# Kernel optimization log

Measured on AMD Instinct MI355X. Metric: run time of the kernel, lower is better.

Reference implementation:

```python
import jax, jax.numpy as jnp
import numpy as np


def setup_inputs() -> dict:
    key = jax.random.key(0)
    k1, k2 = jax.random.split(key)
    B, S, D = 32, 1024, 384
    MAX_MEL_LEN = 8192  # >= max possible sum of durations (7*1024)
    x = jax.random.normal(k1, (B, S, D), dtype=jnp.float32)
    duration = jax.random.randint(k2, (B, S), 0, 8, dtype=jnp.int32)
    return {"x": x, "duration": duration, "max_mel_len": MAX_MEL_LEN}


def reference(x, duration, max_mel_len):
    # x: (B, S, D) float, duration: (B, S) int, max_mel_len: python int
    B, S, D = x.shape
    csum = jnp.cumsum(duration, axis=1)          # (B, S) inclusive cumsum
    mel_len = csum[:, -1]                        # (B,) expanded length per sample
    t = jnp.arange(max_mel_len, dtype=csum.dtype)  # (T,) output frame indices
    # frame t maps to token i where csum[i-1] <= t < csum[i]; side='right'
    # correctly skips zero-duration tokens (repeated csum values)
    idx = jax.vmap(lambda c: jnp.searchsorted(c, t, side='right'))(csum)  # (B, T)
    idx = jnp.clip(idx, 0, S - 1)
    out = jnp.take_along_axis(x, idx[:, :, None], axis=1)  # (B, T, D) gather
    mask = t[None, :] < mel_len[:, None]                   # (B, T) pad mask
    out = out * mask[:, :, None].astype(x.dtype)
    return out, mel_len.astype(jnp.int64)
```

## Files before the change

### kernel.cpp

```cpp
#include <hip/hip_runtime.h>


#define BATCH 32
#define SRC_S 1024
#define DIM   384
#define ROWS  32
#define C4    (DIM / 4)
#define NXCD  8

typedef float f32x4 __attribute__((ext_vector_type(4)));

__global__ void lr_scan_idx_kernel(const int* __restrict__ duration,
                                   int* __restrict__ idx_g,
                                   float* __restrict__ mel_out, int T) {
    __shared__ int wsum[16];
    const int b = blockIdx.x;
    const int tid = threadIdx.x;
    const int lane = tid & 63;
    const int wid = tid >> 6;
    const int d = duration[b * SRC_S + tid];

    int v = d;
    #pragma unroll
    for (int off = 1; off < 64; off <<= 1) {
        const int n = __shfl_up(v, off, 64);
        if (lane >= off) v += n;
    }
    if (lane == 63) wsum[wid] = v;
    __syncthreads();
    if (tid < 16) {
        int w = wsum[tid];
        #pragma unroll
        for (int off = 1; off < 16; off <<= 1) {
            const int n = __shfl_up(w, off, 64);
            if (tid >= off) w += n;
        }
        wsum[tid] = w;
    }
    __syncthreads();
    const int wbase = (wid == 0) ? 0 : wsum[wid - 1];
    const int end = wbase + v;
    const int start = end - d;
    const int mel_len = wsum[15];

    int* __restrict__ ib = idx_g + (size_t)b * T;
    for (int t = start; t < end; ++t) ib[t] = tid;
    for (int t = mel_len + tid; t < T; t += SRC_S) ib[t] = -1;

    if (tid == SRC_S - 1) mel_out[b] = (float)mel_len;
}

__global__ __launch_bounds__(256)
void lr_gather_kernel(const f32x4* __restrict__ x4,
                      const int* __restrict__ idx_g,
                      f32x4* __restrict__ out4, int T) {
    const int l = blockIdx.x;
    const int xcd = l & (NXCD - 1);
    const int j = l >> 3;
    const int b = xcd + NXCD * (j >> 8);
    const int t0 = (j & 255) * ROWS;
    const int tid = threadIdx.x;

    const int* __restrict__ ib = idx_g + (size_t)b * T + t0;
    const f32x4* __restrict__ xb = x4 + (size_t)b * SRC_S * C4;
    f32x4* __restrict__ ob = out4 + ((size_t)b * T + t0) * C4;

    #pragma unroll
    for (int k = 0; k < (ROWS * C4) / 256; ++k) {
        const int i = tid + k * 256;
        const int row = i / C4;
        const int col = i - row * C4;
        const int sidx = ib[row];
        f32x4 v = (f32x4)(0.f);
        if (sidx >= 0) v = xb[(size_t)sidx * C4 + col];
        __builtin_nontemporal_store(v, &ob[i]);
    }
}

extern "C" void kernel_launch(void* const* d_in, const int* in_sizes, int n_in,
                              void* d_out, int out_size, void* d_ws, size_t ws_size,
                              hipStream_t stream) {
    const float* x = (const float*)d_in[0];
    const int* duration = (const int*)d_in[1];
    const int T = (out_size - BATCH) / (BATCH * DIM);

    int* idx_g = (int*)d_ws;
    float* out = (float*)d_out;
    float* mel_out = out + (size_t)BATCH * T * DIM;

    lr_scan_idx_kernel<<<BATCH, SRC_S, 0, stream>>>(duration, idx_g, mel_out, T);

    const int nblocks = BATCH * (T / ROWS);
    lr_gather_kernel<<<nblocks, 256, 0, stream>>>((const f32x4*)x, idx_g,
                                                  (f32x4*)out, T);
}
```

Measured before the change: 438.7 us.

## Fuse duration scan into gather kernel, recompute indices per block in LDS

Removes the separate scan/index-building kernel and its global index buffer. Each gather block now loads the whole duration row for its batch as int4 vectors, computes the prefix sum with wave shuffles, and writes source indices for its 32 output rows into shared memory. This saves one kernel launch and the global index writes and reads, at the cost of redundant scans across the 256 blocks per batch plus an extra barrier before the gather.

```diff
diff --git a/kernel.cpp b/kernel.cpp
--- a/kernel.cpp
+++ b/kernel.cpp
@@ -9,59 +9,58 @@
 #define NXCD  8
 
 typedef float f32x4 __attribute__((ext_vector_type(4)));
-
-__global__ void lr_scan_idx_kernel(const int* __restrict__ duration,
-                                   int* __restrict__ idx_g,
-                                   float* __restrict__ mel_out, int T) {
-    __shared__ int wsum[16];
-    const int b = blockIdx.x;
-    const int tid = threadIdx.x;
-    const int lane = tid & 63;
-    const int wid = tid >> 6;
-    const int d = duration[b * SRC_S + tid];
-
-    int v = d;
-    #pragma unroll
-    for (int off = 1; off < 64; off <<= 1) {
-        const int n = __shfl_up(v, off, 64);
-        if (lane >= off) v += n;
-    }
-    if (lane == 63) wsum[wid] = v;
-    __syncthreads();
-    if (tid < 16) {
-        int w = wsum[tid];
-        #pragma unroll
-        for (int off = 1; off < 16; off <<= 1) {
-            const int n = __shfl_up(w, off, 64);
-            if (tid >= off) w += n;
-        }
-        wsum[tid] = w;
-    }
-    __syncthreads();
-    const int wbase = (wid == 0) ? 0 : wsum[wid - 1];
-    const int end = wbase + v;
-    const int start = end - d;
-    const int mel_len = wsum[15];
-
-    int* __restrict__ ib = idx_g + (size_t)b * T;
-    for (int t = start; t < end; ++t) ib[t] = tid;
-    for (int t = mel_len + tid; t < T; t += SRC_S) ib[t] = -1;
-
-    if (tid == SRC_S - 1) mel_out[b] = (float)mel_len;
-}
+typedef int   i32x4 __attribute__((ext_vector_type(4)));
 
 __global__ __launch_bounds__(256)
-void lr_gather_kernel(const f32x4* __restrict__ x4,
-                      const int* __restrict__ idx_g,
-                      f32x4* __restrict__ out4, int T) {
+void lr_fused_kernel(const f32x4* __restrict__ x4,
+                     const int* __restrict__ duration,
+                     f32x4* __restrict__ out4,
+                     float* __restrict__ mel_out, int T) {
+    __shared__ int wsum[4];
+    __shared__ int src[ROWS];
+
     const int l = blockIdx.x;
     const int xcd = l & (NXCD - 1);
     const int j = l >> 3;
     const int b = xcd + NXCD * (j >> 8);
     const int t0 = (j & 255) * ROWS;
     const int tid = threadIdx.x;
+    const int lane = tid & 63;
+    const int wid = tid >> 6;
 
-    const int* __restrict__ ib = idx_g + (size_t)b * T + t0;
+    if (tid < ROWS) src[tid] = -1;
+
+    const i32x4 d = ((const i32x4*)(duration + b * SRC_S))[tid];
+    const int s0 = d.x;
+    const int s1 = s0 + d.y;
+    const int s2 = s1 + d.z;
+    const int s3 = s2 + d.w;
+    int tot = s3;
+    #pragma unroll
+    for (int off = 1; off < 64; off <<= 1) {
+        const int n = __shfl_up(tot, off, 64);
+        if (lane >= off) tot += n;
+    }
+    if (lane == 63) wsum[wid] = tot;
+    __syncthreads();
+    int base = 0;
+    #pragma unroll
+    for (int w = 0; w < 3; ++w) base += (w < wid) ? wsum[w] : 0;
+    const int mel_len = wsum[0] + wsum[1] + wsum[2] + wsum[3];
+    const int pre = base + tot - s3;
+
+    const int cs[4] = {pre + s0, pre + s1, pre + s2, pre + s3};
+    const int st[4] = {pre, pre + s0, pre + s1, pre + s2};
+    #pragma unroll
+    for (int e = 0; e < 4; ++e) {
+        const int lo = (st[e] > t0) ? st[e] : t0;
+        const int hi = (cs[e] < t0 + ROWS) ? cs[e] : (t0 + ROWS);
+        for (int t = lo; t < hi; ++t) src[t - t0] = tid * 4 + e;
+    }
+    __syncthreads();
+
+    if (t0 == 0 && tid == 0) mel_out[b] = (float)mel_len;
+
     const f32x4* __restrict__ xb = x4 + (size_t)b * SRC_S * C4;
     f32x4* __restrict__ ob = out4 + ((size_t)b * T + t0) * C4;
 
@@ -70,7 +69,7 @@
         const int i = tid + k * 256;
         const int row = i / C4;
         const int col = i - row * C4;
-        const int sidx = ib[row];
+        const int sidx = src[row];
         f32x4 v = (f32x4)(0.f);
         if (sidx >= 0) v = xb[(size_t)sidx * C4 + col];
         __builtin_nontemporal_store(v, &ob[i]);
@@ -84,13 +83,10 @@
     const int* duration = (const int*)d_in[1];
     const int T = (out_size - BATCH) / (BATCH * DIM);
 
-    int* idx_g = (int*)d_ws;
     float* out = (float*)d_out;
     float* mel_out = out + (size_t)BATCH * T * DIM;
 
-    lr_scan_idx_kernel<<<BATCH, SRC_S, 0, stream>>>(duration, idx_g, mel_out, T);
-
     const int nblocks = BATCH * (T / ROWS);
-    lr_gather_kernel<<<nblocks, 256, 0, stream>>>((const f32x4*)x, idx_g,
-                                                  (f32x4*)out, T);
+    lr_fused_kernel<<<nblocks, 256, 0, stream>>>((const f32x4*)x, duration,
+                                                 (f32x4*)out, mel_out, T);
 }
```

Result: no change. 436.0 us (median of 2 runs) (-0.6%).
